# Kernel optimization log

Hardware: AMD Instinct MI355X
Metric: run time of the kernel (lower is better)

## Reference

```python
import jax, jax.numpy as jnp
import numpy as np

N, F_IN, F_OUT = 8192, 512, 256
NEG_BIG = -9e15


def setup_inputs() -> dict:
    key = jax.random.key(0)
    k1, k2, k3, k4, k5 = jax.random.split(key, 5)
    h = jax.random.normal(k1, (N, F_IN), dtype=jnp.float32)
    adj = jax.random.randint(k2, (N, N), 0, 2, dtype=jnp.int32)
    W = jax.random.normal(k3, (F_IN, F_OUT), dtype=jnp.float32) / np.sqrt(F_IN)
    bW = jnp.zeros((F_OUT,), dtype=jnp.float32)
    a1 = jax.random.normal(k4, (F_OUT,), dtype=jnp.float32) / np.sqrt(2 * F_OUT)
    a2 = jax.random.normal(k5, (F_OUT,), dtype=jnp.float32) / np.sqrt(2 * F_OUT)
    ba = jnp.zeros((), dtype=jnp.float32)
    return {"h": h, "adj": adj, "W": W, "bW": bW, "a1": a1, "a2": a2, "ba": ba}


def reference(h, adj, W, bW, a1, a2, ba):
    # Wh: [N, F_OUT]
    Wh = h @ W + bW
    # a([Wh_i ; Wh_j]) + b == (Wh_i . a1) + (Wh_j . a2) + b  (rank-1 decomposition,
    # avoids the O(N^2 * 2F) repeat/cat tensor the torch code materializes)
    f1 = Wh @ a1  # [N]
    f2 = Wh @ a2  # [N]
    e = jax.nn.leaky_relu(f1[:, None] + f2[None, :] + ba, negative_slope=0.2)
    e = jnp.where(adj > 0, e, NEG_BIG)
    attention = jax.nn.softmax(e, axis=1)  # dropout = identity (eval mode)
    return attention @ Wh
```

## Files before the change

kernel.cpp:

```cpp
#include <hip/hip_runtime.h>

typedef __bf16 bf16;
typedef __attribute__((ext_vector_type(4))) float f32x4;
typedef __attribute__((ext_vector_type(8))) __bf16 bf16x8;
typedef __attribute__((ext_vector_type(4))) __bf16 bf16x4;
typedef __attribute__((ext_vector_type(4))) int i32x4;

#define NN 8192
#define FI 512
#define FO 256
#define NSPLIT 4
#define JCHUNK (NN / NSPLIT)

__global__ __launch_bounds__(256) void kw_split(const float* __restrict__ W,
                                                bf16* __restrict__ wth,
                                                bf16* __restrict__ wtl) {
  const int idx = blockIdx.x * 256 + threadIdx.x;
  const int k = idx >> 8, n = idx & 255;
  float x = W[idx];
  bf16 hi = (bf16)x;
  wth[(size_t)n * FI + k] = hi;
  wtl[(size_t)n * FI + k] = (bf16)(x - (float)hi);
}

__global__ __launch_bounds__(256) void k1_gemm(
    const float* __restrict__ h, const bf16* __restrict__ wth,
    const bf16* __restrict__ wtl, const float* __restrict__ bW,
    const float* __restrict__ a1, const float* __restrict__ a2,
    bf16* __restrict__ whb, float* __restrict__ f1, float* __restrict__ f2) {
  __shared__ bf16 stg[32 * 256];
  const int t = threadIdx.x;
  const int lane = t & 63, w = t >> 6;
  const int m16 = lane & 15, q = lane >> 4;
  const int wr = w & 1, wn = w >> 1;
  const int rb = blockIdx.x;
  const int row = rb * 32 + wr * 16 + m16;
  const int nb = wn * 128;

  const f32x4 z4 = {0.f, 0.f, 0.f, 0.f};
  f32x4 acc[8];
#pragma unroll
  for (int nn = 0; nn < 8; ++nn) acc[nn] = z4;

  const float* hrow = h + (size_t)row * FI + q * 8;
  const bf16* wthp = wth + (size_t)(nb + m16) * FI + q * 8;
  const bf16* wtlp = wtl + (size_t)(nb + m16) * FI + q * 8;

  for (int kt = 0; kt < FI / 32; ++kt) {
    f32x4 h0 = *(const f32x4*)(hrow + kt * 32);
    f32x4 h1 = *(const f32x4*)(hrow + kt * 32 + 4);
    bf16x8 hh, hl;
#pragma unroll
    for (int x = 0; x < 4; ++x) {
      float v = h0[x];
      bf16 hi = (bf16)v;
      hh[x] = hi;
      hl[x] = (bf16)(v - (float)hi);
      float v2 = h1[x];
      bf16 hi2 = (bf16)v2;
      hh[4 + x] = hi2;
      hl[4 + x] = (bf16)(v2 - (float)hi2);
    }
#pragma unroll
    for (int nn = 0; nn < 8; ++nn) {
      const size_t woff = (size_t)(nn * 16) * FI + kt * 32;
      bf16x8 bh = *(const bf16x8*)(wthp + woff);
      bf16x8 bl = *(const bf16x8*)(wtlp + woff);
      acc[nn] = __builtin_amdgcn_mfma_f32_16x16x32_bf16(hh, bh, acc[nn], 0, 0, 0);
      acc[nn] = __builtin_amdgcn_mfma_f32_16x16x32_bf16(hl, bh, acc[nn], 0, 0, 0);
      acc[nn] = __builtin_amdgcn_mfma_f32_16x16x32_bf16(hh, bl, acc[nn], 0, 0, 0);
    }
  }
  float f1p[4] = {}, f2p[4] = {};
  const int il = wr * 16 + q * 4;
#pragma unroll
  for (int nn = 0; nn < 8; ++nn) {
    const int n = nb + nn * 16 + m16;
    const float bw = bW[n], av1 = a1[n], av2 = a2[n];
#pragma unroll
    for (int reg = 0; reg < 4; ++reg) {
      float wh = acc[nn][reg] + bw;
      stg[n * 32 + il + reg] = (bf16)wh;
      f1p[reg] += wh * av1;
      f2p[reg] += wh * av2;
    }
  }
#pragma unroll
  for (int m = 1; m < 16; m <<= 1) {
#pragma unroll
    for (int reg = 0; reg < 4; ++reg) {
      f1p[reg] += __shfl_xor(f1p[reg], m);
      f2p[reg] += __shfl_xor(f2p[reg], m);
    }
  }
  if (m16 == 0) {
#pragma unroll
    for (int reg = 0; reg < 4; ++reg) {
      const int i = rb * 32 + wr * 16 + q * 4 + reg;
      atomicAdd(&f1[i], f1p[reg]);
      atomicAdd(&f2[i], f2p[reg]);
    }
  }
  __syncthreads();
  bf16x8* dst = (bf16x8*)(whb + (size_t)rb * (FO * 32));
  const bf16x8* srcv = (const bf16x8*)stg;
#pragma unroll
  for (int u = 0; u < 4; ++u) dst[t * 4 + u] = srcv[t * 4 + u];
}

__global__ __launch_bounds__(256, 4) void k4_attn(
    const int* __restrict__ adj, const bf16* __restrict__ whb,
    const float* __restrict__ f1, const float* __restrict__ f2,
    const float* __restrict__ ba_p,
    float* __restrict__ acc_part, float* __restrict__ l_part) {
  const int t = threadIdx.x;
  const int lane = t & 63, w = t >> 6;
  const int m16 = lane & 15, q = lane >> 4;
  const int wr = w & 1, wn = w >> 1;
  const int rb = blockIdx.x, s = blockIdx.y;
  const int i0 = rb * 32;
  const int row = i0 + wr * 16 + m16;

  const float ba = *ba_p;
  const float ci = f1[row] + ba;
  const float arg0 = ci + 8.0f;
  const float sh = fmaxf(arg0, 0.2f * arg0);

  const f32x4 z4 = {0.f, 0.f, 0.f, 0.f};
  f32x4 acc[8];
#pragma unroll
  for (int nn = 0; nn < 8; ++nn) acc[nn] = z4;
  float lreg = 0.f;

  const int sbase = s * JCHUNK;
  const int* arow = adj + (size_t)row * NN + sbase + q * 8;
  const float* frow = f2 + sbase + q * 8;
  const bf16* bptr = whb + (size_t)(sbase >> 5) * (FO * 32) +
                     (size_t)(wn * 128 + m16) * 32 + q * 8;

  i32x4 na0 = *(const i32x4*)(arow);
  i32x4 na1 = *(const i32x4*)(arow + 4);
  f32x4 nf0 = *(const f32x4*)(frow);
  f32x4 nf1 = *(const f32x4*)(frow + 4);

  const int KT = JCHUNK / 32;
  for (int kt = 0; kt < KT; ++kt) {
    const i32x4 ca0 = na0;
    const i32x4 ca1 = na1;
    const f32x4 cf0 = nf0;
    const f32x4 cf1 = nf1;
    if (kt + 1 < KT) {
      na0 = *(const i32x4*)(arow + (kt + 1) * 32);
      na1 = *(const i32x4*)(arow + (kt + 1) * 32 + 4);
      nf0 = *(const f32x4*)(frow + (kt + 1) * 32);
      nf1 = *(const f32x4*)(frow + (kt + 1) * 32 + 4);
    }
    float pv[8];
#pragma unroll
    for (int x = 0; x < 4; ++x) {
      float arg = ci + cf0[x];
      float e = fmaxf(arg, 0.2f * arg);
      pv[x] = (ca0[x] > 0) ? __expf(e - sh) : 0.f;
      float arg2 = ci + cf1[x];
      float e2 = fmaxf(arg2, 0.2f * arg2);
      pv[4 + x] = (ca1[x] > 0) ? __expf(e2 - sh) : 0.f;
    }
    bf16x8 af;
#pragma unroll
    for (int x = 0; x < 8; ++x) {
      lreg += pv[x];
      af[x] = (bf16)pv[x];
    }
    const bf16* bk = bptr + (size_t)kt * (FO * 32);
#pragma unroll
    for (int nn = 0; nn < 8; ++nn) {
      bf16x8 bfr = *(const bf16x8*)(bk + nn * (16 * 32));
      acc[nn] = __builtin_amdgcn_mfma_f32_16x16x32_bf16(af, bfr, acc[nn], 0, 0, 0);
    }
  }
  lreg += __shfl_xor(lreg, 16);
  lreg += __shfl_xor(lreg, 32);
  if (q == 0 && wn == 0) l_part[(size_t)s * NN + row] = lreg;
  float* ap = acc_part + (size_t)s * ((size_t)NN * FO);
  const int r0 = i0 + wr * 16 + q * 4;
#pragma unroll
  for (int nn = 0; nn < 8; ++nn) {
    const int n = wn * 128 + nn * 16 + m16;
#pragma unroll
    for (int reg = 0; reg < 4; ++reg) {
      ap[(size_t)(r0 + reg) * FO + n] = acc[nn][reg];
    }
  }
}

__global__ __launch_bounds__(256) void k5_reduce(
    const float* __restrict__ accp, const float* __restrict__ lp,
    float* __restrict__ out) {
  const int idx = blockIdx.x * 256 + threadIdx.x;
  const int i = idx >> 6, n4 = (idx & 63) * 4;
  f32x4 sum = {0.f, 0.f, 0.f, 0.f};
  float l = 0.f;
#pragma unroll
  for (int s = 0; s < NSPLIT; ++s) {
    sum += *(const f32x4*)&accp[(size_t)s * ((size_t)NN * FO) + (size_t)i * FO + n4];
    l += lp[s * NN + i];
  }
  const float rl = 1.0f / l;
  f32x4 o = sum * rl;
  *(f32x4*)&out[(size_t)i * FO + n4] = o;
}

extern "C" void kernel_launch(void* const* d_in, const int* in_sizes, int n_in,
                              void* d_out, int out_size, void* d_ws, size_t ws_size,
                              hipStream_t stream) {
  const float* h   = (const float*)d_in[0];
  const int*   adj = (const int*)d_in[1];
  const float* W   = (const float*)d_in[2];
  const float* bW  = (const float*)d_in[3];
  const float* a1  = (const float*)d_in[4];
  const float* a2  = (const float*)d_in[5];
  const float* ba  = (const float*)d_in[6];
  float* out = (float*)d_out;

  char* ws = (char*)d_ws;
  bf16* whb   = (bf16*)ws;
  float* f1   = (float*)(ws + 4u * 1024 * 1024);
  float* f2   = (float*)(ws + 4u * 1024 * 1024 + 32 * 1024);
  float* accp = (float*)(ws + 4u * 1024 * 1024 + 64 * 1024);
  float* lp   = accp + (size_t)NSPLIT * NN * FO;
  bf16* wth   = (bf16*)((char*)lp + (size_t)NSPLIT * NN * 4);
  bf16* wtl   = wth + (size_t)FO * FI;

  hipMemsetAsync(f1, 0, 64 * 1024, stream);

  kw_split<<<FI * FO / 256, 256, 0, stream>>>(W, wth, wtl);
  k1_gemm<<<NN / 32, 256, 0, stream>>>(h, wth, wtl, bW, a1, a2, whb, f1, f2);
  k4_attn<<<dim3(NN / 32, NSPLIT), 256, 0, stream>>>(adj, whb, f1, f2, ba, accp, lp);
  k5_reduce<<<(NN * FO / 4) / 256, 256, 0, stream>>>(accp, lp, out);
}
```

Measured before the change: 569.5 us.

## Split GEMM output columns across blocks and hoist B-fragment loads ahead of compute

The feature GEMM now launches twice as many blocks, each covering 128 output columns instead of 256, with a smaller accumulator set and launch bounds asking for two blocks per CU. It also prefetches the next h tile and issues all weight loads before the MFMAs. In the attention kernel, the Wh B-fragment loads for each step are moved before the exp/mask computation so their latency overlaps the ALU work, and the adjacency prefetch is made unconditional by clamping the index. The cost is higher register pressure, h rows being reread by both column blocks, and one redundant load on the last iteration.

```diff
diff --git a/kernel.cpp b/kernel.cpp
--- a/kernel.cpp
+++ b/kernel.cpp
@@ -23,32 +23,45 @@
   wtl[(size_t)n * FI + k] = (bf16)(x - (float)hi);
 }
 
-__global__ __launch_bounds__(256) void k1_gemm(
+__global__ __launch_bounds__(256, 2) void k1_gemm(
     const float* __restrict__ h, const bf16* __restrict__ wth,
     const bf16* __restrict__ wtl, const float* __restrict__ bW,
     const float* __restrict__ a1, const float* __restrict__ a2,
     bf16* __restrict__ whb, float* __restrict__ f1, float* __restrict__ f2) {
-  __shared__ bf16 stg[32 * 256];
+  __shared__ bf16 stg[128 * 32];
   const int t = threadIdx.x;
   const int lane = t & 63, w = t >> 6;
   const int m16 = lane & 15, q = lane >> 4;
   const int wr = w & 1, wn = w >> 1;
-  const int rb = blockIdx.x;
+  const int rb = blockIdx.x, bj = blockIdx.y;
   const int row = rb * 32 + wr * 16 + m16;
-  const int nb = wn * 128;
+  const int nb = bj * 128 + wn * 64;
 
   const f32x4 z4 = {0.f, 0.f, 0.f, 0.f};
-  f32x4 acc[8];
-#pragma unroll
-  for (int nn = 0; nn < 8; ++nn) acc[nn] = z4;
+  f32x4 acc[4];
+#pragma unroll
+  for (int nn = 0; nn < 4; ++nn) acc[nn] = z4;
 
   const float* hrow = h + (size_t)row * FI + q * 8;
   const bf16* wthp = wth + (size_t)(nb + m16) * FI + q * 8;
   const bf16* wtlp = wtl + (size_t)(nb + m16) * FI + q * 8;
 
-  for (int kt = 0; kt < FI / 32; ++kt) {
-    f32x4 h0 = *(const f32x4*)(hrow + kt * 32);
-    f32x4 h1 = *(const f32x4*)(hrow + kt * 32 + 4);
+  f32x4 nh0 = *(const f32x4*)(hrow);
+  f32x4 nh1 = *(const f32x4*)(hrow + 4);
+
+  const int KT = FI / 32;
+  for (int kt = 0; kt < KT; ++kt) {
+    bf16x8 bh[4], bl[4];
+#pragma unroll
+    for (int nn = 0; nn < 4; ++nn) {
+      const size_t woff = (size_t)(nn * 16) * FI + kt * 32;
+      bh[nn] = *(const bf16x8*)(wthp + woff);
+      bl[nn] = *(const bf16x8*)(wtlp + woff);
+    }
+    const f32x4 h0 = nh0, h1 = nh1;
+    const int ktn = (kt + 1 < KT) ? kt + 1 : kt;
+    nh0 = *(const f32x4*)(hrow + ktn * 32);
+    nh1 = *(const f32x4*)(hrow + ktn * 32 + 4);
     bf16x8 hh, hl;
 #pragma unroll
     for (int x = 0; x < 4; ++x) {
@@ -62,28 +75,28 @@
       hl[4 + x] = (bf16)(v2 - (float)hi2);
     }
 #pragma unroll
-    for (int nn = 0; nn < 8; ++nn) {
-      const size_t woff = (size_t)(nn * 16) * FI + kt * 32;
-      bf16x8 bh = *(const bf16x8*)(wthp + woff);
-      bf16x8 bl = *(const bf16x8*)(wtlp + woff);
-      acc[nn] = __builtin_amdgcn_mfma_f32_16x16x32_bf16(hh, bh, acc[nn], 0, 0, 0);
-      acc[nn] = __builtin_amdgcn_mfma_f32_16x16x32_bf16(hl, bh, acc[nn], 0, 0, 0);
-      acc[nn] = __builtin_amdgcn_mfma_f32_16x16x32_bf16(hh, bl, acc[nn], 0, 0, 0);
+    for (int nn = 0; nn < 4; ++nn) {
+      acc[nn] = __builtin_amdgcn_mfma_f32_16x16x32_bf16(hh, bh[nn], acc[nn], 0, 0, 0);
+      acc[nn] = __builtin_amdgcn_mfma_f32_16x16x32_bf16(hl, bh[nn], acc[nn], 0, 0, 0);
+      acc[nn] = __builtin_amdgcn_mfma_f32_16x16x32_bf16(hh, bl[nn], acc[nn], 0, 0, 0);
     }
   }
   float f1p[4] = {}, f2p[4] = {};
   const int il = wr * 16 + q * 4;
 #pragma unroll
-  for (int nn = 0; nn < 8; ++nn) {
+  for (int nn = 0; nn < 4; ++nn) {
     const int n = nb + nn * 16 + m16;
+    const int nl = wn * 64 + nn * 16 + m16;
     const float bw = bW[n], av1 = a1[n], av2 = a2[n];
+    bf16x4 st;
 #pragma unroll
     for (int reg = 0; reg < 4; ++reg) {
       float wh = acc[nn][reg] + bw;
-      stg[n * 32 + il + reg] = (bf16)wh;
+      st[reg] = (bf16)wh;
       f1p[reg] += wh * av1;
       f2p[reg] += wh * av2;
     }
+    *(bf16x4*)&stg[nl * 32 + il] = st;
   }
 #pragma unroll
   for (int m = 1; m < 16; m <<= 1) {
@@ -102,10 +115,10 @@
     }
   }
   __syncthreads();
-  bf16x8* dst = (bf16x8*)(whb + (size_t)rb * (FO * 32));
+  bf16x8* dst = (bf16x8*)(whb + (size_t)rb * (FO * 32) + (size_t)bj * (128 * 32));
   const bf16x8* srcv = (const bf16x8*)stg;
 #pragma unroll
-  for (int u = 0; u < 4; ++u) dst[t * 4 + u] = srcv[t * 4 + u];
+  for (int u = 0; u < 2; ++u) dst[t * 2 + u] = srcv[t * 2 + u];
 }
 
 __global__ __launch_bounds__(256, 4) void k4_attn(
@@ -145,16 +158,20 @@
 
   const int KT = JCHUNK / 32;
   for (int kt = 0; kt < KT; ++kt) {
+    bf16x8 cb[8];
+    const bf16* bk = bptr + (size_t)kt * (FO * 32);
+#pragma unroll
+    for (int nn = 0; nn < 8; ++nn)
+      cb[nn] = *(const bf16x8*)(bk + nn * (16 * 32));
     const i32x4 ca0 = na0;
     const i32x4 ca1 = na1;
     const f32x4 cf0 = nf0;
     const f32x4 cf1 = nf1;
-    if (kt + 1 < KT) {
-      na0 = *(const i32x4*)(arow + (kt + 1) * 32);
-      na1 = *(const i32x4*)(arow + (kt + 1) * 32 + 4);
-      nf0 = *(const f32x4*)(frow + (kt + 1) * 32);
-      nf1 = *(const f32x4*)(frow + (kt + 1) * 32 + 4);
-    }
+    const int ktn = (kt + 1 < KT) ? kt + 1 : kt;
+    na0 = *(const i32x4*)(arow + ktn * 32);
+    na1 = *(const i32x4*)(arow + ktn * 32 + 4);
+    nf0 = *(const f32x4*)(frow + ktn * 32);
+    nf1 = *(const f32x4*)(frow + ktn * 32 + 4);
     float pv[8];
 #pragma unroll
     for (int x = 0; x < 4; ++x) {
@@ -171,12 +188,9 @@
       lreg += pv[x];
       af[x] = (bf16)pv[x];
     }
-    const bf16* bk = bptr + (size_t)kt * (FO * 32);
-#pragma unroll
-    for (int nn = 0; nn < 8; ++nn) {
-      bf16x8 bfr = *(const bf16x8*)(bk + nn * (16 * 32));
-      acc[nn] = __builtin_amdgcn_mfma_f32_16x16x32_bf16(af, bfr, acc[nn], 0, 0, 0);
-    }
+#pragma unroll
+    for (int nn = 0; nn < 8; ++nn)
+      acc[nn] = __builtin_amdgcn_mfma_f32_16x16x32_bf16(af, cb[nn], acc[nn], 0, 0, 0);
   }
   lreg += __shfl_xor(lreg, 16);
   lreg += __shfl_xor(lreg, 32);
@@ -234,7 +248,7 @@
   hipMemsetAsync(f1, 0, 64 * 1024, stream);
 
   kw_split<<<FI * FO / 256, 256, 0, stream>>>(W, wth, wtl);
-  k1_gemm<<<NN / 32, 256, 0, stream>>>(h, wth, wtl, bW, a1, a2, whb, f1, f2);
+  k1_gemm<<<dim3(NN / 32, 2), 256, 0, stream>>>(h, wth, wtl, bW, a1, a2, whb, f1, f2);
   k4_attn<<<dim3(NN / 32, NSPLIT), 256, 0, stream>>>(adj, whb, f1, f2, ba, accp, lp);
   k5_reduce<<<(NN * FO / 4) / 256, 256, 0, stream>>>(accp, lp, out);
 }
```

Result: no change. 559.0 us (-1.9%).
